# Optimization experiments

Measured on AMD Instinct MI355X. Metric: run time of the kernel, lower is better.

The kernel has to match this reference:

```python
import jax, jax.numpy as jnp
import numpy as np

B, S, E, A = 4, 4096, 512, 64

def setup_inputs() -> dict:
    key = jax.random.key(0)
    ks = jax.random.split(key, 9)
    return {
        "query": jax.random.normal(ks[0], (B, S, E), dtype=jnp.float32),
        "key":   jax.random.normal(ks[1], (B, S, E), dtype=jnp.float32),
        "value": jax.random.normal(ks[2], (B, S, E), dtype=jnp.float32),
        "Wq": jax.random.normal(ks[3], (E, A), dtype=jnp.float32) / np.sqrt(E),
        "bq": jax.random.normal(ks[4], (A,), dtype=jnp.float32) * 0.01,
        "Wk": jax.random.normal(ks[5], (E, A), dtype=jnp.float32) / np.sqrt(E),
        "bk": jax.random.normal(ks[6], (A,), dtype=jnp.float32) * 0.01,
        "Wv": jax.random.normal(ks[7], (E, A), dtype=jnp.float32) / np.sqrt(E),
        "bv": jax.random.normal(ks[8], (A,), dtype=jnp.float32) * 0.01,
        "look_ahead_mask": 1,
    }

def reference(query, key, value, Wq, bq, Wk, bk, Wv, bv, look_ahead_mask):
    # Linear projections (torch Linear: x @ W^T + b; here W stored as [in,out])
    q = query @ Wq + bq            # [B,S,A]
    k = key   @ Wk + bk            # [B,S,A]
    v = value @ Wv + bv            # [B,S,A]
    scale = jnp.sqrt(jnp.asarray(A, dtype=q.dtype))
    qk = jnp.einsum('bsa,bta->bst', q, k) / scale   # [B,S,S]
    if look_ahead_mask:
        # faithful to source: MULTIPLICATIVE tril mask (not additive -inf)
        tril = jnp.tril(jnp.ones((qk.shape[-1], qk.shape[-1]), dtype=qk.dtype))
        qk = qk * tril
    attn = jax.nn.softmax(qk, axis=-1)              # [B,S,S]
    return jnp.einsum('bst,bta->bsa', attn, v)       # [B,S,A]
```

## Files before the change

### kernel.cpp

```cpp
#include <hip/hip_runtime.h>
#include <cstdint>

constexpr int BB = 4, SS = 4096, EE = 512, AA = 64;
constexpr int NT = 64;
constexpr int NSLOT = 272;
constexpr int TSH = 12288;

typedef __bf16 bf16x8 __attribute__((ext_vector_type(8)));
typedef float  f32x4  __attribute__((ext_vector_type(4)));
typedef float  f4     __attribute__((ext_vector_type(4)));
typedef unsigned short u16x4 __attribute__((ext_vector_type(4)));
typedef unsigned short u16x8 __attribute__((ext_vector_type(8)));

#define MFMA16(a, b, c) __builtin_amdgcn_mfma_f32_16x16x32_bf16((a), (b), (c), 0, 0, 0)

typedef const void __attribute__((address_space(1))) gvoid_t;
typedef void __attribute__((address_space(3))) lvoid_t;
__device__ __forceinline__ void gload16(const void* g, void* l) {
    __builtin_amdgcn_global_load_lds((gvoid_t*)g, (lvoid_t*)l, 16, 0, 0);
}

__device__ __forceinline__ unsigned short f2bf(float x) {
    union { float f; unsigned u; } v; v.f = x;
    unsigned r = v.u + 0x7fffu + ((v.u >> 16) & 1u);
    return (unsigned short)(r >> 16);
}
__device__ __forceinline__ float bf2f(unsigned short h) {
    union { unsigned u; float f; } v; v.u = ((unsigned)h) << 16;
    return v.f;
}
__device__ __forceinline__ unsigned short f2bfc(float x) {
    __bf16 h = (__bf16)x;
    return __builtin_bit_cast(unsigned short, h);
}
__device__ __forceinline__ bf16x8 as_bf16x8(u16x8 u) {
    union { u16x8 u; bf16x8 b; } v; v.u = u; return v.b;
}

__global__ void split_w_kernel(const float* __restrict__ Wq,
                               const float* __restrict__ Wk,
                               const float* __restrict__ Wv,
                               unsigned short* __restrict__ wt_h,
                               unsigned short* __restrict__ wt_l) {
    int idx = blockIdx.x * blockDim.x + threadIdx.x;
    if (idx >= 3 * EE * AA) return;
    int t = idx / (EE * AA);
    int rem = idx - t * (EE * AA);
    int k = rem >> 6;
    int n = rem & 63;
    const float* W = (t == 0) ? Wq : (t == 1) ? Wk : Wv;
    float x = W[k * AA + n];
    unsigned short h = f2bf(x);
    unsigned short l = f2bf(x - bf2f(h));
    int o = (t * AA + n) * EE + k;
    wt_h[o] = h;
    wt_l[o] = l;
}

__launch_bounds__(128)
__global__ void proj_kernel(const float* __restrict__ Xq,
                            const float* __restrict__ Xk,
                            const float* __restrict__ Xv,
                            const float* __restrict__ bq,
                            const float* __restrict__ bk,
                            const float* __restrict__ bv,
                            const unsigned short* __restrict__ wt_h,
                            const unsigned short* __restrict__ wt_l,
                            unsigned short* __restrict__ q_hi,
                            unsigned short* __restrict__ q_lo,
                            unsigned short* __restrict__ kv) {
    const int t = blockIdx.y;
    const float* X    = (t == 0) ? Xq : (t == 1) ? Xk : Xv;
    const float* bias = (t == 0) ? bq : (t == 1) ? bk : bv;
    const int row0 = blockIdx.x * 32;
    const int tid = threadIdx.x;
    const int lane = tid & 63, w = tid >> 6;
    const int l15 = lane & 15, l4 = lane >> 4;

    __shared__ __align__(16) char smem[24576];

    f32x4 acc[4];
#pragma unroll
    for (int j = 0; j < 4; ++j) acc[j] = (f32x4){0.f, 0.f, 0.f, 0.f};

    const unsigned short* wtH = wt_h + t * AA * EE;
    const unsigned short* wtL = wt_l + t * AA * EE;

    for (int kc0 = 0; kc0 < EE; kc0 += 64) {
#pragma unroll
        for (int s = 0; s < 4; ++s) {
            int r = s * 8 + (tid >> 4);
            int c4 = (tid & 15) ^ (r & 7);
            gload16(X + (size_t)(row0 + r) * EE + kc0 + c4 * 4,
                    smem + s * 2048 + tid * 16);
        }
#pragma unroll
        for (int s = 0; s < 4; ++s) {
            int n = s * 16 + (tid >> 3);
            int cg = (tid & 7) ^ (n & 7);
            gload16(wtH + n * EE + kc0 + cg * 8,
                    smem + 8192 + s * 2048 + tid * 16);
            gload16(wtL + n * EE + kc0 + cg * 8,
                    smem + 16384 + s * 2048 + tid * 16);
        }
        asm volatile("s_waitcnt vmcnt(0)" ::: "memory");
        __syncthreads();

#pragma unroll
        for (int kc = 0; kc < 2; ++kc) {
            int r = w * 16 + l15;
            int c4a = (kc * 8 + l4 * 2) ^ (r & 7);
            int c4b = (kc * 8 + l4 * 2 + 1) ^ (r & 7);
            f4 va = *(const f4*)(smem + r * 256 + c4a * 16);
            f4 vb = *(const f4*)(smem + r * 256 + c4b * 16);
            u16x8 ahu, alu;
#pragma unroll
            for (int jj = 0; jj < 4; ++jj) {
                __bf16 h0 = (__bf16)va[jj];
                ahu[jj] = __builtin_bit_cast(unsigned short, h0);
                alu[jj] = f2bfc(va[jj] - (float)h0);
                __bf16 h1 = (__bf16)vb[jj];
                ahu[jj + 4] = __builtin_bit_cast(unsigned short, h1);
                alu[jj + 4] = f2bfc(vb[jj] - (float)h1);
            }
            bf16x8 a_h = as_bf16x8(ahu), a_l = as_bf16x8(alu);
#pragma unroll
            for (int j = 0; j < 4; ++j) {
                int n = j * 16 + l15;
                int byteB = n * 128 + (((kc * 4 + l4) ^ (n & 7)) << 4);
                bf16x8 b_h = as_bf16x8(*(const u16x8*)(smem + 8192 + byteB));
                bf16x8 b_l = as_bf16x8(*(const u16x8*)(smem + 16384 + byteB));
                acc[j] = MFMA16(a_h, b_h, acc[j]);
                acc[j] = MFMA16(a_h, b_l, acc[j]);
                acc[j] = MFMA16(a_l, b_h, acc[j]);
            }
        }
        __syncthreads();
    }

    float* stage = (float*)smem;
#pragma unroll
    for (int j = 0; j < 4; ++j) {
        int n = j * 16 + l15;
        float bv_ = bias[n];
#pragma unroll
        for (int reg = 0; reg < 4; ++reg) {
            int r = w * 16 + l4 * 4 + reg;
            stage[r * 65 + n] = acc[j][reg] + bv_;
        }
    }
    __syncthreads();

    if (t == 0) {
        int row = tid >> 2, n0 = (tid & 3) * 16;
        u16x8 h0, l0, h1, l1;
#pragma unroll
        for (int k = 0; k < 8; ++k) {
            float v = stage[row * 65 + n0 + k] * 0.125f;
            __bf16 hh = (__bf16)v;
            h0[k] = __builtin_bit_cast(unsigned short, hh);
            l0[k] = f2bfc(v - (float)hh);
        }
#pragma unroll
        for (int k = 0; k < 8; ++k) {
            float v = stage[row * 65 + n0 + 8 + k] * 0.125f;
            __bf16 hh = (__bf16)v;
            h1[k] = __builtin_bit_cast(unsigned short, hh);
            l1[k] = f2bfc(v - (float)hh);
        }
        size_t o = (size_t)(row0 + row) * AA + n0;
        *(u16x8*)(q_hi + o) = h0; *(u16x8*)(q_hi + o + 8) = h1;
        *(u16x8*)(q_lo + o) = l0; *(u16x8*)(q_lo + o + 8) = l1;
    } else if (t == 1) {
        const int bb = row0 >> 12, kt = (row0 & 4095) >> 6;
        const int hb = (row0 >> 5) & 1;
        const size_t base = (size_t)(bb * NT + kt) * TSH;
        const int ff = tid >> 5;
#pragma unroll
        for (int p = 0; p < 2; ++p) {
            int lane2 = (tid & 31) * 2 + p;
            int f = (ff >> 1) * 4 + 2 * hb + (ff & 1);
            int n0 = (f >> 2) * 32 + (lane2 >> 4) * 8;
            int tt = (f & 3) * 16 + (lane2 & 15);
            int sr = tt & 31;
            u16x8 h;
#pragma unroll
            for (int jj = 0; jj < 8; ++jj)
                h[jj] = f2bfc(stage[sr * 65 + n0 + jj]);
            *(u16x8*)(kv + base + (size_t)f * 512 + lane2 * 8) = h;
        }
    } else {
        const int bb = row0 >> 12, kt = (row0 & 4095) >> 6;
        const int hb = (row0 >> 5) & 1;
        const size_t base = (size_t)(bb * NT + kt) * TSH + 4096;
        const int ff = tid >> 5;
#pragma unroll
        for (int p = 0; p < 2; ++p) {
            int lane2 = (tid & 31) * 2 + p;
            int f = 4 * hb + ff;
            int n = (f & 3) * 16 + (lane2 & 15);
            int tt0 = (lane2 >> 4) * 8;
            u16x8 h, l;
#pragma unroll
            for (int jj = 0; jj < 8; ++jj) {
                float v = stage[(tt0 + jj) * 65 + n];
                __bf16 hh = (__bf16)v;
                h[jj] = __builtin_bit_cast(unsigned short, hh);
                l[jj] = f2bfc(v - (float)hh);
            }
            size_t o = base + (size_t)f * 512 + lane2 * 8;
            *(u16x8*)(kv + o) = h;
            *(u16x8*)(kv + o + 4096) = l;
        }
    }
}

__launch_bounds__(64)
__global__ void sufv_kernel(const unsigned short* __restrict__ kv,
                            float* __restrict__ sufv) {
    const int b = blockIdx.x >> 6;
    const int a = blockIdx.x & 63;
    const int t = threadIdx.x;
    __shared__ float sums[64];
    const size_t tb = (size_t)(b * NT + t) * TSH + 4096;
    const int j = a >> 4, l15i = a & 15;
    float s = 0.f;
#pragma unroll
    for (int c2 = 0; c2 < 2; ++c2) {
#pragma unroll
        for (int l4i = 0; l4i < 4; ++l4i) {
            size_t off = tb + (((c2 * 4 + j) * 64 + l4i * 16 + l15i) << 3);
            u16x8 h = *(const u16x8*)(kv + off);
            u16x8 l = *(const u16x8*)(kv + off + 4096);
#pragma unroll
            for (int q = 0; q < 8; ++q) s += bf2f(h[q]) + bf2f(l[q]);
        }
    }
    sums[t] = s;
    __syncthreads();
    float suf = 0.f;
    for (int jj = t + 1; jj < 64; ++jj) suf += sums[jj];
    sufv[((size_t)(b * 64 + a)) * 64 + t] = suf;
}

__launch_bounds__(512)
__global__ void attn_chunk_kernel(const unsigned short* __restrict__ q_hi,
                                  const unsigned short* __restrict__ q_lo,
                                  const unsigned short* __restrict__ kv,
                                  float* __restrict__ facc_part,
                                  float* __restrict__ l_part) {
    const int idx = (int)blockIdx.x;
    const int b = idx & 3;
    const int s = (NSLOT - 1) - (idx >> 2);
    int k = (int)sqrtf((float)s + 0.5f);
    while (k * k > s) --k;
    while ((k + 1) * (k + 1) <= s) ++k;
    int i, c;
    if (s < k * (k + 1)) { i = 2 * k - 1; c = s - k * k; }
    else                 { i = 2 * k;     c = s - k * (k + 1); }
    const int t_begin = c * 4;
    const int tmax = 2 * i + 2;
    const int t_end = (t_begin + 4 < tmax) ? t_begin + 4 : tmax;

    const int tid = threadIdx.x;
    const int lane = tid & 63, w = tid >> 6;
    const int l15 = lane & 15, l4 = lane >> 4;

    __shared__ __align__(16) unsigned short kvbuf[TSH];
    __shared__ __align__(16) unsigned short plds[8][1024];

    bf16x8 qh[2], ql[2];
    {
        size_t qrow = (size_t)(b * SS + i * 128 + w * 16 + l15) * AA;
#pragma unroll
        for (int kc = 0; kc < 2; ++kc) {
            qh[kc] = as_bf16x8(*(const u16x8*)(q_hi + qrow + kc * 32 + l4 * 8));
            ql[kc] = as_bf16x8(*(const u16x8*)(q_lo + qrow + kc * 32 + l4 * 8));
        }
    }

    f32x4 facc[4];
#pragma unroll
    for (int j = 0; j < 4; ++j) facc[j] = (f32x4){0.f, 0.f, 0.f, 0.f};
    float lsum = 0.f;

    const char* lb = (const char*)kvbuf;
    const int qbase = i * 128 + w * 16;
    const char* gbase = (const char*)kv + (size_t)(b * NT) * (TSH * 2) + tid * 16;

    for (int kt = t_begin; kt < t_end; ++kt) {
        {
            const char* gt = gbase + (size_t)kt * (TSH * 2);
            char* lw = (char*)kvbuf + tid * 16;
#pragma unroll
            for (int p = 0; p < 3; ++p) gload16(gt + p * 8192, lw + p * 8192);
        }
        asm volatile("s_waitcnt vmcnt(0)" ::: "memory");
        __syncthreads();

        f32x4 sc[4];
#pragma unroll
        for (int j = 0; j < 4; ++j) sc[j] = (f32x4){0.f, 0.f, 0.f, 0.f};
        __builtin_amdgcn_s_setprio(1);
#pragma unroll
        for (int kc = 0; kc < 2; ++kc) {
#pragma unroll
            for (int j2 = 0; j2 < 4; ++j2) {
                int f = kc * 4 + j2;
                bf16x8 h = as_bf16x8(*(const u16x8*)(lb + f * 1024 + lane * 16));
                sc[j2] = MFMA16(h, qh[kc], sc[j2]);
                sc[j2] = MFMA16(h, ql[kc], sc[j2]);
            }
        }
        __builtin_amdgcn_s_setprio(0);

        const int dq = qbase - 64 * kt;
        const bool anyMask = (dq < 63);
#pragma unroll
        for (int j2 = 0; j2 < 4; ++j2) {
            u16x4 p4;
#pragma unroll
            for (int reg = 0; reg < 4; ++reg) {
                float sv_ = sc[j2][reg];
                if (anyMask) {
                    int tl = j2 * 16 + l4 * 4 + reg;
                    if (tl > dq + l15) sv_ = 0.f;
                }
                float p = __expf(sv_);
                lsum += p;
                p4[reg] = f2bf(p);
            }
            int byte = (l15 * 128 + j2 * 32 + l4 * 8) ^ ((l15 & 7) << 4);
            *(u16x4*)((char*)plds[w] + byte) = p4;
        }

        __builtin_amdgcn_s_setprio(1);
#pragma unroll
        for (int c2 = 0; c2 < 2; ++c2) {
            int byteA = (l15 * 128 + c2 * 64 + l4 * 16) ^ ((l15 & 7) << 4);
            bf16x8 pf = as_bf16x8(*(const u16x8*)((const char*)plds[w] + byteA));
#pragma unroll
            for (int j = 0; j < 4; ++j) {
                int f = c2 * 4 + j;
                bf16x8 vh = as_bf16x8(*(const u16x8*)(lb + 8192 + f * 1024 + lane * 16));
                bf16x8 vl = as_bf16x8(*(const u16x8*)(lb + 16384 + f * 1024 + lane * 16));
                facc[j] = MFMA16(pf, vh, facc[j]);
                facc[j] = MFMA16(pf, vl, facc[j]);
            }
        }
        __builtin_amdgcn_s_setprio(0);

        if (kt + 1 < t_end) __syncthreads();
    }

    {
        float rs = lsum;
        rs += __shfl_xor(rs, 16);
        rs += __shfl_xor(rs, 32);
        const size_t slot = (size_t)b * NSLOT + s;
        if (l4 == 0)
            l_part[slot * 128 + w * 16 + l15] = rs;

        float* fp = facc_part + slot * 8192;
#pragma unroll
        for (int j = 0; j < 4; ++j) {
#pragma unroll
            for (int reg = 0; reg < 4; ++reg) {
                int row = w * 16 + l4 * 4 + reg, a = j * 16 + l15;
                fp[row * 64 + a] = facc[j][reg];
            }
        }
    }
}

__launch_bounds__(256)
__global__ void combine_kernel(const float* __restrict__ facc_part,
                               const float* __restrict__ l_part,
                               const float* __restrict__ sufv,
                               float* __restrict__ out) {
    const int i64 = blockIdx.x;
    const int b = blockIdx.y;
    const int tid = threadIdx.x;
    const int i128 = i64 >> 1;
    const int nch = (i128 >> 1) + 1;
    const int k2 = i128 >> 1;
    const int C = (i128 & 1) ? (k2 + 1) * (k2 + 1) : k2 * (k2 + 1);
    const size_t slot0 = (size_t)b * NSLOT + C;
    const int rbase = (i64 & 1) * 64;
    __shared__ float linv[64];
    __shared__ float sv[64];
    if (tid < 64) {
        float l = 64.0f * (float)(NT - 2 * i128 - 2);
        for (int cc = 0; cc < nch; ++cc)
            l += l_part[(slot0 + cc) * 128 + rbase + tid];
        linv[tid] = 1.f / l;
        sv[tid] = sufv[((size_t)(b * 64 + tid)) * 64 + (2 * i128 + 1)];
    }
    __syncthreads();
    float* ob = out + ((size_t)(b * SS + i64 * 64)) * AA;
#pragma unroll
    for (int k = 0; k < 4; ++k) {
        int e = (tid + k * 256) * 4;
        int row = e >> 6, a = e & 63;
        f4 acc = {sv[a], sv[a + 1], sv[a + 2], sv[a + 3]};
        for (int cc = 0; cc < nch; ++cc) {
            f4 v = *(const f4*)(facc_part + (slot0 + cc) * 8192 + (rbase + row) * 64 + a);
            acc += v;
        }
        acc *= linv[row];
        *(f4*)(ob + e) = acc;
    }
}

extern "C" void kernel_launch(void* const* d_in, const int* in_sizes, int n_in,
                              void* d_out, int out_size, void* d_ws, size_t ws_size,
                              hipStream_t stream) {
    const float* query = (const float*)d_in[0];
    const float* key   = (const float*)d_in[1];
    const float* value = (const float*)d_in[2];
    const float* Wq    = (const float*)d_in[3];
    const float* bq    = (const float*)d_in[4];
    const float* Wk    = (const float*)d_in[5];
    const float* bk    = (const float*)d_in[6];
    const float* Wv    = (const float*)d_in[7];
    const float* bv    = (const float*)d_in[8];

    char* ws = (char*)d_ws;
    const size_t MB = 1u << 20;
    unsigned short* q_hi = (unsigned short*)(ws + 0 * MB);
    unsigned short* q_lo = (unsigned short*)(ws + 2 * MB);
    unsigned short* kv   = (unsigned short*)(ws + 4 * MB);
    float* sufv      = (float*)(ws + 12 * MB);
    float* l_part    = (float*)(ws + 13 * MB);
    float* facc_part = (float*)(ws + 14 * MB);
    unsigned short* wt_h = (unsigned short*)(ws + 52 * MB);
    unsigned short* wt_l = wt_h + 3 * AA * EE;

    split_w_kernel<<<(3 * EE * AA + 255) / 256, 256, 0, stream>>>(Wq, Wk, Wv, wt_h, wt_l);
    proj_kernel<<<dim3(BB * SS / 32, 3), 128, 0, stream>>>(
        query, key, value, bq, bk, bv, wt_h, wt_l, q_hi, q_lo, kv);
    sufv_kernel<<<BB * AA, 64, 0, stream>>>(kv, sufv);
    attn_chunk_kernel<<<dim3(4 * NSLOT, 1), 512, 0, stream>>>(
        q_hi, q_lo, kv, facc_part, l_part);
    combine_kernel<<<dim3(NT, BB), 256, 0, stream>>>(facc_part, l_part, sufv, (float*)d_out);
}
```

Measured before the change: 90.46 us.

## Restructure projection tiling with direct X loads and store partial accumulators as bf16

The projection kernel now processes 64 rows per 256-thread block. Each lane loads its X row slice straight from global memory into registers, and LDS holds only the hi/lo weight halves for a 256-wide K range, staged in two phases instead of eight 64-wide chunks. The K/V layout writes drop the half-block indexing to match the larger tile. Separately, the attention partial accumulators are written as bf16 instead of fp32 and widened back in the combine kernel, halving that intermediate's traffic. The bf16 partials reduce output accuracy, and the larger LDS footprint (64 KB) limits occupancy.

```diff
diff --git a/kernel.cpp b/kernel.cpp
--- a/kernel.cpp
+++ b/kernel.cpp
@@ -57,7 +57,7 @@
     wt_l[o] = l;
 }
 
-__launch_bounds__(128)
+__launch_bounds__(256, 2)
 __global__ void proj_kernel(const float* __restrict__ Xq,
                             const float* __restrict__ Xk,
                             const float* __restrict__ Xv,
@@ -72,12 +72,12 @@
     const int t = blockIdx.y;
     const float* X    = (t == 0) ? Xq : (t == 1) ? Xk : Xv;
     const float* bias = (t == 0) ? bq : (t == 1) ? bk : bv;
-    const int row0 = blockIdx.x * 32;
+    const int row0 = blockIdx.x * 64;
     const int tid = threadIdx.x;
     const int lane = tid & 63, w = tid >> 6;
     const int l15 = lane & 15, l4 = lane >> 4;
 
-    __shared__ __align__(16) char smem[24576];
+    __shared__ __align__(16) char smem[65536];
 
     f32x4 acc[4];
 #pragma unroll
@@ -85,34 +85,32 @@
 
     const unsigned short* wtH = wt_h + t * AA * EE;
     const unsigned short* wtL = wt_l + t * AA * EE;
-
-    for (int kc0 = 0; kc0 < EE; kc0 += 64) {
-#pragma unroll
-        for (int s = 0; s < 4; ++s) {
-            int r = s * 8 + (tid >> 4);
-            int c4 = (tid & 15) ^ (r & 7);
-            gload16(X + (size_t)(row0 + r) * EE + kc0 + c4 * 4,
-                    smem + s * 2048 + tid * 16);
-        }
-#pragma unroll
-        for (int s = 0; s < 4; ++s) {
-            int n = s * 16 + (tid >> 3);
-            int cg = (tid & 7) ^ (n & 7);
-            gload16(wtH + n * EE + kc0 + cg * 8,
-                    smem + 8192 + s * 2048 + tid * 16);
-            gload16(wtL + n * EE + kc0 + cg * 8,
-                    smem + 16384 + s * 2048 + tid * 16);
+    const float* xrow = X + (size_t)(row0 + w * 16 + l15) * EE + l4 * 8;
+
+#pragma unroll
+    for (int ph = 0; ph < 2; ++ph) {
+        const int kh = ph * 256;
+#pragma unroll
+        for (int s8 = 0; s8 < 8; ++s8) {
+            int e = s8 * 256 + tid;
+            int n = e >> 5, g = e & 31;
+            int cg = g ^ (n & 7);
+            gload16(wtH + n * EE + kh + cg * 8, smem + e * 16);
+            gload16(wtL + n * EE + kh + cg * 8, smem + 32768 + e * 16);
         }
         asm volatile("s_waitcnt vmcnt(0)" ::: "memory");
         __syncthreads();
 
-#pragma unroll
-        for (int kc = 0; kc < 2; ++kc) {
-            int r = w * 16 + l15;
-            int c4a = (kc * 8 + l4 * 2) ^ (r & 7);
-            int c4b = (kc * 8 + l4 * 2 + 1) ^ (r & 7);
-            f4 va = *(const f4*)(smem + r * 256 + c4a * 16);
-            f4 vb = *(const f4*)(smem + r * 256 + c4b * 16);
+        f4 xv[16];
+#pragma unroll
+        for (int kq = 0; kq < 8; ++kq) {
+            xv[2 * kq]     = *(const f4*)(xrow + kh + kq * 32);
+            xv[2 * kq + 1] = *(const f4*)(xrow + kh + kq * 32 + 4);
+        }
+
+#pragma unroll
+        for (int kq = 0; kq < 8; ++kq) {
+            f4 va = xv[2 * kq], vb = xv[2 * kq + 1];
             u16x8 ahu, alu;
 #pragma unroll
             for (int jj = 0; jj < 4; ++jj) {
@@ -127,9 +125,9 @@
 #pragma unroll
             for (int j = 0; j < 4; ++j) {
                 int n = j * 16 + l15;
-                int byteB = n * 128 + (((kc * 4 + l4) ^ (n & 7)) << 4);
-                bf16x8 b_h = as_bf16x8(*(const u16x8*)(smem + 8192 + byteB));
-                bf16x8 b_l = as_bf16x8(*(const u16x8*)(smem + 16384 + byteB));
+                int byteB = n * 512 + (((kq * 4 + l4) ^ (n & 7)) << 4);
+                bf16x8 b_h = as_bf16x8(*(const u16x8*)(smem + byteB));
+                bf16x8 b_l = as_bf16x8(*(const u16x8*)(smem + 32768 + byteB));
                 acc[j] = MFMA16(a_h, b_h, acc[j]);
                 acc[j] = MFMA16(a_h, b_l, acc[j]);
                 acc[j] = MFMA16(a_l, b_h, acc[j]);
@@ -173,33 +171,28 @@
         *(u16x8*)(q_lo + o) = l0; *(u16x8*)(q_lo + o + 8) = l1;
     } else if (t == 1) {
         const int bb = row0 >> 12, kt = (row0 & 4095) >> 6;
-        const int hb = (row0 >> 5) & 1;
         const size_t base = (size_t)(bb * NT + kt) * TSH;
-        const int ff = tid >> 5;
+        const int f = tid >> 5;
 #pragma unroll
         for (int p = 0; p < 2; ++p) {
             int lane2 = (tid & 31) * 2 + p;
-            int f = (ff >> 1) * 4 + 2 * hb + (ff & 1);
             int n0 = (f >> 2) * 32 + (lane2 >> 4) * 8;
             int tt = (f & 3) * 16 + (lane2 & 15);
-            int sr = tt & 31;
             u16x8 h;
 #pragma unroll
             for (int jj = 0; jj < 8; ++jj)
-                h[jj] = f2bfc(stage[sr * 65 + n0 + jj]);
+                h[jj] = f2bfc(stage[tt * 65 + n0 + jj]);
             *(u16x8*)(kv + base + (size_t)f * 512 + lane2 * 8) = h;
         }
     } else {
         const int bb = row0 >> 12, kt = (row0 & 4095) >> 6;
-        const int hb = (row0 >> 5) & 1;
         const size_t base = (size_t)(bb * NT + kt) * TSH + 4096;
-        const int ff = tid >> 5;
+        const int f = tid >> 5;
 #pragma unroll
         for (int p = 0; p < 2; ++p) {
             int lane2 = (tid & 31) * 2 + p;
-            int f = 4 * hb + ff;
             int n = (f & 3) * 16 + (lane2 & 15);
-            int tt0 = (lane2 >> 4) * 8;
+            int tt0 = (f >> 2) * 32 + (lane2 >> 4) * 8;
             u16x8 h, l;
 #pragma unroll
             for (int jj = 0; jj < 8; ++jj) {
@@ -247,7 +240,7 @@
 __global__ void attn_chunk_kernel(const unsigned short* __restrict__ q_hi,
                                   const unsigned short* __restrict__ q_lo,
                                   const unsigned short* __restrict__ kv,
-                                  float* __restrict__ facc_part,
+                                  unsigned short* __restrict__ facc_part,
                                   float* __restrict__ l_part) {
     const int idx = (int)blockIdx.x;
     const int b = idx & 3;
@@ -361,20 +354,20 @@
         if (l4 == 0)
             l_part[slot * 128 + w * 16 + l15] = rs;
 
-        float* fp = facc_part + slot * 8192;
+        unsigned short* fp = facc_part + slot * 8192;
 #pragma unroll
         for (int j = 0; j < 4; ++j) {
 #pragma unroll
             for (int reg = 0; reg < 4; ++reg) {
                 int row = w * 16 + l4 * 4 + reg, a = j * 16 + l15;
-                fp[row * 64 + a] = facc[j][reg];
+                fp[row * 64 + a] = f2bfc(facc[j][reg]);
             }
         }
     }
 }
 
 __launch_bounds__(256)
-__global__ void combine_kernel(const float* __restrict__ facc_part,
+__global__ void combine_kernel(const unsigned short* __restrict__ facc_part,
                                const float* __restrict__ l_part,
                                const float* __restrict__ sufv,
                                float* __restrict__ out) {
@@ -404,8 +397,12 @@
         int row = e >> 6, a = e & 63;
         f4 acc = {sv[a], sv[a + 1], sv[a + 2], sv[a + 3]};
         for (int cc = 0; cc < nch; ++cc) {
-            f4 v = *(const f4*)(facc_part + (slot0 + cc) * 8192 + (rbase + row) * 64 + a);
-            acc += v;
+            u16x4 r4 = *(const u16x4*)(facc_part + (slot0 + cc) * 8192 +
+                                       (rbase + row) * 64 + a);
+            acc[0] += bf2f(r4[0]);
+            acc[1] += bf2f(r4[1]);
+            acc[2] += bf2f(r4[2]);
+            acc[3] += bf2f(r4[3]);
         }
         acc *= linv[row];
         *(f4*)(ob + e) = acc;
@@ -432,12 +429,12 @@
     unsigned short* kv   = (unsigned short*)(ws + 4 * MB);
     float* sufv      = (float*)(ws + 12 * MB);
     float* l_part    = (float*)(ws + 13 * MB);
-    float* facc_part = (float*)(ws + 14 * MB);
+    unsigned short* facc_part = (unsigned short*)(ws + 14 * MB);
     unsigned short* wt_h = (unsigned short*)(ws + 52 * MB);
     unsigned short* wt_l = wt_h + 3 * AA * EE;
 
     split_w_kernel<<<(3 * EE * AA + 255) / 256, 256, 0, stream>>>(Wq, Wk, Wv, wt_h, wt_l);
-    proj_kernel<<<dim3(BB * SS / 32, 3), 128, 0, stream>>>(
+    proj_kernel<<<dim3(BB * SS / 64, 3), 256, 0, stream>>>(
         query, key, value, bq, bk, bv, wt_h, wt_l, q_hi, q_lo, kv);
     sufv_kernel<<<BB * AA, 64, 0, stream>>>(kv, sufv);
     attn_chunk_kernel<<<dim3(4 * NSLOT, 1), 512, 0, stream>>>(
```

Result: slower. 99.46 us (+9.9%).
